# Kernel optimization log

Measured on AMD Instinct MI355X. Metric: run time of the kernel, lower is better.

Reference implementation:

```python
import jax, jax.numpy as jnp
import numpy as np


def setup_inputs() -> dict:
    key = jax.random.key(0)
    ks = jax.random.split(key, 7)
    B, Din, H = 65536, 256, 512
    s_in = 1.0 / np.sqrt(Din)
    s_h = 1.0 / np.sqrt(H)
    return {
        "input_x": jax.random.normal(ks[0], (B, Din), jnp.float32),
        "h_old": jax.random.normal(ks[1], (B, H), jnp.float32),
        "c_old": jax.random.normal(ks[2], (B, H), jnp.float32),
        # stacked gate weights, order [i, f, o, c]
        "U": jax.random.normal(ks[3], (4, Din, H), jnp.float32) * s_in,
        "bU": jnp.zeros((4, H), jnp.float32),
        "W": jax.random.normal(ks[4], (4, H, H), jnp.float32) * s_h,
        "bW": jnp.zeros((4, H), jnp.float32),
    }


def reference(input_x, h_old, c_old, U, bU, W, bW):
    # Two fused GEMMs over all four gates: [B, 4, H]
    gx = jnp.einsum('bd,gdh->bgh', input_x, U) + bU[None, :, :]
    gh = jnp.einsum('bh,ghk->bgk', h_old, W) + bW[None, :, :]
    g = gx + gh  # [B, 4, H], gate order i, f, o, c
    i_t = jax.nn.sigmoid(g[:, 0])
    f_t = jax.nn.sigmoid(g[:, 1])
    o_t = jax.nn.sigmoid(g[:, 2])
    c_t = jnp.tanh(g[:, 3])
    c_new = i_t * c_t + f_t * c_old
    h_new = o_t * jnp.tanh(c_new)
    return (h_new, c_new)
```

## Files before the change

kernel.cpp:

```cpp
#include <hip/hip_runtime.h>
#include <stdint.h>
#include <stddef.h>

#define BATCH 65536
#define DIN   256
#define HDIM  512
#define KDIM  768
#define NDIM  2048
#define HN_ELEMS (BATCH * HDIM)

using f32x4 = __attribute__((ext_vector_type(4))) float;
using s16x8 = __attribute__((ext_vector_type(8))) short;
using u16x8 = __attribute__((ext_vector_type(8))) unsigned short;

__device__ __forceinline__ unsigned short f2bf(float f) {
    union { float f; unsigned u; } v; v.f = f;
    unsigned r = v.u + 0x7fffu + ((v.u >> 16) & 1u);
    return (unsigned short)(r >> 16);
}

__global__ __launch_bounds__(256) void pack_a_kernel(
    const float* __restrict__ x, const float* __restrict__ h,
    unsigned short* __restrict__ aPack)
{
    int idx = blockIdx.x * 256 + threadIdx.x;
    int row = idx / 96;
    int seg = idx - row * 96;
    const float* src = (seg < 32) ? (x + (size_t)row * DIN  + seg * 8)
                                  : (h + (size_t)row * HDIM + (seg - 32) * 8);
    const f32x4* s4 = (const f32x4*)src;
    f32x4 v0 = s4[0], v1 = s4[1];
    u16x8 o;
    o[0] = f2bf(v0[0]); o[1] = f2bf(v0[1]); o[2] = f2bf(v0[2]); o[3] = f2bf(v0[3]);
    o[4] = f2bf(v1[0]); o[5] = f2bf(v1[1]); o[6] = f2bf(v1[2]); o[7] = f2bf(v1[3]);
    *(u16x8*)(aPack + (size_t)row * KDIM + seg * 8) = o;
}

__global__ __launch_bounds__(256) void pack_w_kernel(
    const float* __restrict__ U, const float* __restrict__ W,
    unsigned short* __restrict__ wPack)
{
    int t = blockIdx.x * 256 + threadIdx.x;
    int k = t >> 11;
    int n = t & 2047;
    int g = (n >> 4) & 3;
    int h = ((n >> 6) << 4) | (n & 15);
    float v = (k < DIN) ? U[((size_t)g * DIN  + k)        * HDIM + h]
                        : W[((size_t)g * HDIM + (k - DIN)) * HDIM + h];
    wPack[(size_t)n * KDIM + k] = f2bf(v);
}

__global__ __launch_bounds__(256) void pack_bias_kernel(
    const float* __restrict__ bU, const float* __restrict__ bW,
    float* __restrict__ bias)
{
    int n = blockIdx.x * 256 + threadIdx.x;
    int g = (n >> 4) & 3;
    int h = ((n >> 6) << 4) | (n & 15);
    bias[n] = bU[g * HDIM + h] + bW[g * HDIM + h];
}

__global__ __launch_bounds__(256) void lstm_gemm_kernel(
    const unsigned short* __restrict__ aPack,
    const unsigned short* __restrict__ wPack,
    const float* __restrict__ bias,
    const float* __restrict__ c_old,
    float* __restrict__ out)
{
    __shared__ __align__(16) unsigned short smem[8192];

    const int tid = threadIdx.x;
    const int w   = tid >> 6;
    const int l   = tid & 63;
    const int bx  = blockIdx.x;
    const int n0  = (bx & 15) * 128;
    const int m0  = (bx >> 4) * 128;
    const int wm  = w >> 1;
    const int wn  = w & 1;
    const int lq  = l >> 4;
    const int lc  = l & 15;

    f32x4 acc[4][4];
#pragma unroll
    for (int i = 0; i < 4; ++i)
#pragma unroll
        for (int j = 0; j < 4; ++j)
            acc[i][j] = (f32x4){0.f, 0.f, 0.f, 0.f};

    const int stg_row = w * 16 + (l >> 2);
    const int stg_col = (l & 3) * 8;

    for (int kt = 0; kt < 24; ++kt) {
        const int k0 = kt * 32;
#pragma unroll
        for (int j = 0; j < 2; ++j) {
            const int r = stg_row + j * 64;
            const unsigned short* ga = aPack + (size_t)(m0 + r) * KDIM + k0 + stg_col;
            const unsigned short* gb = wPack + (size_t)(n0 + r) * KDIM + k0 + stg_col;
            unsigned short* la = &smem[(j * 4 + w) * 512];
            unsigned short* lb = &smem[4096 + (j * 4 + w) * 512];
            __builtin_amdgcn_global_load_lds(
                (const __attribute__((address_space(1))) void*)ga,
                (__attribute__((address_space(3))) void*)la, 16, 0, 0);
            __builtin_amdgcn_global_load_lds(
                (const __attribute__((address_space(1))) void*)gb,
                (__attribute__((address_space(3))) void*)lb, 16, 0, 0);
        }
        __syncthreads();

        s16x8 af[4], bf[4];
#pragma unroll
        for (int i = 0; i < 4; ++i) {
            int row = wm * 64 + i * 16 + lc;
            af[i] = *(const s16x8*)&smem[row * 32 + lq * 8];
        }
#pragma unroll
        for (int j = 0; j < 4; ++j) {
            int row = wn * 64 + j * 16 + lc;
            bf[j] = *(const s16x8*)&smem[4096 + row * 32 + lq * 8];
        }
#pragma unroll
        for (int i = 0; i < 4; ++i)
#pragma unroll
            for (int j = 0; j < 4; ++j)
                acc[i][j] = __builtin_amdgcn_mfma_f32_16x16x32_bf16(af[i], bf[j], acc[i][j], 0, 0, 0);
        __syncthreads();
    }

    const int nbase = n0 + wn * 64;
    const int hcol  = (nbase >> 2) + lc;
    const float b0 = bias[nbase +  0 + lc];
    const float b1 = bias[nbase + 16 + lc];
    const float b2 = bias[nbase + 32 + lc];
    const float b3 = bias[nbase + 48 + lc];

#pragma unroll
    for (int i = 0; i < 4; ++i) {
        const int rowb = m0 + wm * 64 + i * 16 + lq * 4;
#pragma unroll
        for (int r = 0; r < 4; ++r) {
            const int row = rowb + r;
            const float gi = acc[i][0][r] + b0;
            const float gf = acc[i][1][r] + b1;
            const float go = acc[i][2][r] + b2;
            const float gc = acc[i][3][r] + b3;
            const float it = 1.f / (1.f + __expf(-gi));
            const float ft = 1.f / (1.f + __expf(-gf));
            const float ot = 1.f / (1.f + __expf(-go));
            const float ct = 2.f / (1.f + __expf(-2.f * gc)) - 1.f;
            const float co = c_old[(size_t)row * HDIM + hcol];
            const float cn = it * ct + ft * co;
            const float tc = 2.f / (1.f + __expf(-2.f * cn)) - 1.f;
            out[(size_t)row * HDIM + hcol] = ot * tc;
            out[(size_t)HN_ELEMS + (size_t)row * HDIM + hcol] = cn;
        }
    }
}

extern "C" void kernel_launch(void* const* d_in, const int* in_sizes, int n_in,
                              void* d_out, int out_size, void* d_ws, size_t ws_size,
                              hipStream_t stream)
{
    const float* x     = (const float*)d_in[0];
    const float* h_old = (const float*)d_in[1];
    const float* c_old = (const float*)d_in[2];
    const float* U     = (const float*)d_in[3];
    const float* bU    = (const float*)d_in[4];
    const float* W     = (const float*)d_in[5];
    const float* bW    = (const float*)d_in[6];
    float* out = (float*)d_out;

    unsigned short* aPack = (unsigned short*)d_ws;
    unsigned short* wPack = (unsigned short*)((char*)d_ws + (size_t)BATCH * KDIM * 2);
    float* bias = (float*)((char*)wPack + (size_t)NDIM * KDIM * 2);

    pack_a_kernel<<<dim3(24576), dim3(256), 0, stream>>>(x, h_old, aPack);
    pack_w_kernel<<<dim3(6144), dim3(256), 0, stream>>>(U, W, wPack);
    pack_bias_kernel<<<dim3(8), dim3(256), 0, stream>>>(bU, bW, bias);
    lstm_gemm_kernel<<<dim3(8192), dim3(256), 0, stream>>>(aPack, wPack, bias, c_old, out);
}
```

Measured before the change: 834.6 us.

## Swizzle LDS tiles, prefetch c_old, stage epilogue stores through LDS, vectorize weight pack

Each thread in the weight pack kernel now packs 8 consecutive K values into one 16-byte store, so the grid is smaller and writes are no longer scattered per element. The GEMM applies an XOR swizzle to the LDS staging columns and fragment reads to reduce bank conflicts. c_old and bias are loaded before the K loop so their latency overlaps the GEMM. The epilogue transposes h_new and c_new through shared memory so each row is written with coalesced 16-byte stores, at the cost of extra barriers and LDS traffic.

```diff
diff --git a/kernel.cpp b/kernel.cpp
--- a/kernel.cpp
+++ b/kernel.cpp
@@ -40,14 +40,23 @@
     const float* __restrict__ U, const float* __restrict__ W,
     unsigned short* __restrict__ wPack)
 {
-    int t = blockIdx.x * 256 + threadIdx.x;
-    int k = t >> 11;
-    int n = t & 2047;
+    int idx = blockIdx.x * 256 + threadIdx.x;
+    int n = idx / 96;
+    int seg = idx - n * 96;
+    int k0 = seg * 8;
     int g = (n >> 4) & 3;
     int h = ((n >> 6) << 4) | (n & 15);
-    float v = (k < DIN) ? U[((size_t)g * DIN  + k)        * HDIM + h]
-                        : W[((size_t)g * HDIM + (k - DIN)) * HDIM + h];
-    wPack[(size_t)n * KDIM + k] = f2bf(v);
+    u16x8 o;
+    if (k0 < DIN) {
+        const float* src = U + ((size_t)g * DIN + k0) * HDIM + h;
+#pragma unroll
+        for (int kk = 0; kk < 8; ++kk) o[kk] = f2bf(src[(size_t)kk * HDIM]);
+    } else {
+        const float* src = W + ((size_t)g * HDIM + (k0 - DIN)) * HDIM + h;
+#pragma unroll
+        for (int kk = 0; kk < 8; ++kk) o[kk] = f2bf(src[(size_t)kk * HDIM]);
+    }
+    *(u16x8*)(wPack + (size_t)n * KDIM + k0) = o;
 }
 
 __global__ __launch_bounds__(256) void pack_bias_kernel(
@@ -80,6 +89,19 @@
     const int lq  = l >> 4;
     const int lc  = l & 15;
 
+    const int nbase = n0 + wn * 64;
+    const int hcol  = (n0 >> 2) + wn * 16 + lc;
+    const float b0 = bias[nbase +  0 + lc];
+    const float b1 = bias[nbase + 16 + lc];
+    const float b2 = bias[nbase + 32 + lc];
+    const float b3 = bias[nbase + 48 + lc];
+    float co[4][4];
+#pragma unroll
+    for (int i = 0; i < 4; ++i)
+#pragma unroll
+        for (int r = 0; r < 4; ++r)
+            co[i][r] = c_old[(size_t)(m0 + wm * 64 + i * 16 + lq * 4 + r) * HDIM + hcol];
+
     f32x4 acc[4][4];
 #pragma unroll
     for (int i = 0; i < 4; ++i)
@@ -88,7 +110,8 @@
             acc[i][j] = (f32x4){0.f, 0.f, 0.f, 0.f};
 
     const int stg_row = w * 16 + (l >> 2);
-    const int stg_col = (l & 3) * 8;
+    const int stg_col = (((l & 3) ^ ((l >> 4) & 3))) * 8;
+    const int swz = (lc >> 2) & 3;
 
     for (int kt = 0; kt < 24; ++kt) {
         const int k0 = kt * 32;
@@ -112,12 +135,12 @@
 #pragma unroll
         for (int i = 0; i < 4; ++i) {
             int row = wm * 64 + i * 16 + lc;
-            af[i] = *(const s16x8*)&smem[row * 32 + lq * 8];
+            af[i] = *(const s16x8*)&smem[row * 32 + (lq ^ swz) * 8];
         }
 #pragma unroll
         for (int j = 0; j < 4; ++j) {
             int row = wn * 64 + j * 16 + lc;
-            bf[j] = *(const s16x8*)&smem[4096 + row * 32 + lq * 8];
+            bf[j] = *(const s16x8*)&smem[4096 + row * 32 + (lq ^ swz) * 8];
         }
 #pragma unroll
         for (int i = 0; i < 4; ++i)
@@ -127,19 +150,15 @@
         __syncthreads();
     }
 
-    const int nbase = n0 + wn * 64;
-    const int hcol  = (nbase >> 2) + lc;
-    const float b0 = bias[nbase +  0 + lc];
-    const float b1 = bias[nbase + 16 + lc];
-    const float b2 = bias[nbase + 32 + lc];
-    const float b3 = bias[nbase + 48 + lc];
+    float* fsm  = (float*)smem;
+    float* hn_t = fsm;
+    float* cn_t = fsm + 1152;
 
 #pragma unroll
     for (int i = 0; i < 4; ++i) {
-        const int rowb = m0 + wm * 64 + i * 16 + lq * 4;
+        f32x4 hnv, cnv;
 #pragma unroll
         for (int r = 0; r < 4; ++r) {
-            const int row = rowb + r;
             const float gi = acc[i][0][r] + b0;
             const float gf = acc[i][1][r] + b1;
             const float go = acc[i][2][r] + b2;
@@ -148,11 +167,31 @@
             const float ft = 1.f / (1.f + __expf(-gf));
             const float ot = 1.f / (1.f + __expf(-go));
             const float ct = 2.f / (1.f + __expf(-2.f * gc)) - 1.f;
-            const float co = c_old[(size_t)row * HDIM + hcol];
-            const float cn = it * ct + ft * co;
+            const float cn = it * ct + ft * co[i][r];
             const float tc = 2.f / (1.f + __expf(-2.f * cn)) - 1.f;
-            out[(size_t)row * HDIM + hcol] = ot * tc;
-            out[(size_t)HN_ELEMS + (size_t)row * HDIM + hcol] = cn;
+            cnv[r] = cn;
+            hnv[r] = ot * tc;
+        }
+        __syncthreads();
+        {
+            const int addr = (wn * 16 + lc) * 36 + wm * 16 + lq * 4;
+            *(f32x4*)&hn_t[addr] = hnv;
+            *(f32x4*)&cn_t[addr] = cnv;
+        }
+        __syncthreads();
+        {
+            const int rloc = tid >> 3;
+            const int cg   = tid & 7;
+            const int grow = m0 + (rloc >> 4) * 64 + i * 16 + (rloc & 15);
+            f32x4 hv, cv;
+#pragma unroll
+            for (int c = 0; c < 4; ++c) {
+                hv[c] = hn_t[(cg * 4 + c) * 36 + rloc];
+                cv[c] = cn_t[(cg * 4 + c) * 36 + rloc];
+            }
+            const size_t ob = (size_t)grow * HDIM + (n0 >> 2) + cg * 4;
+            *(f32x4*)&out[ob] = hv;
+            *(f32x4*)&out[(size_t)HN_ELEMS + ob] = cv;
         }
     }
 }
@@ -175,7 +214,7 @@
     float* bias = (float*)((char*)wPack + (size_t)NDIM * KDIM * 2);
 
     pack_a_kernel<<<dim3(24576), dim3(256), 0, stream>>>(x, h_old, aPack);
-    pack_w_kernel<<<dim3(6144), dim3(256), 0, stream>>>(U, W, wPack);
+    pack_w_kernel<<<dim3(768), dim3(256), 0, stream>>>(U, W, wPack);
     pack_bias_kernel<<<dim3(8), dim3(256), 0, stream>>>(bU, bW, bias);
     lstm_gemm_kernel<<<dim3(8192), dim3(256), 0, stream>>>(aPack, wPack, bias, c_old, out);
 }
```

Result: faster. 755.8 us (-9.4%).
